# Optimization experiments

Hardware: AMD Instinct MI355X
Metric: run time of the kernel (lower is better)

The kernel has to match this reference:

```python
import jax, jax.numpy as jnp
import numpy as np

N = 50000


def gcn_conv(x, edge_index, W, b):
    # x: [N, F_in], edge_index: [2, E] (row=source j, col=target i)
    n = x.shape[0]
    loops = jnp.arange(n, dtype=edge_index.dtype)
    row = jnp.concatenate([edge_index[0], loops])
    col = jnp.concatenate([edge_index[1], loops])
    # linear transform first (PyG GCNConv)
    xw = x @ W  # [N, F_out]
    # symmetric normalization deg^{-1/2}[row] * deg^{-1/2}[col]
    deg = jax.ops.segment_sum(jnp.ones_like(col, dtype=xw.dtype), col, num_segments=n)
    dis = jnp.where(deg > 0, jax.lax.rsqrt(jnp.maximum(deg, 1e-12)), 0.0)
    norm = dis[row] * dis[col]  # [E+N]
    # gather-scale-scatter: sum_j norm_ij * (W x_j)
    msgs = xw[row] * norm[:, None]
    out = jax.ops.segment_sum(msgs, col, num_segments=n)
    return out + b


def setup_inputs() -> dict:
    key = jax.random.key(0)
    k1, k2, k3, k4, k5 = jax.random.split(key, 5)
    in_dim, hidden_dim, out_dim = 128, 128, 64
    x = jax.random.normal(k1, (N, in_dim), dtype=jnp.float32)
    edge_index = jax.random.randint(k2, (2, 800000), 0, N, dtype=jnp.int64)
    s1 = 1.0 / np.sqrt(in_dim)
    s2 = 1.0 / np.sqrt(hidden_dim)
    W1 = jax.random.uniform(k3, (in_dim, hidden_dim), jnp.float32, -s1, s1)
    b1 = jnp.zeros((hidden_dim,), jnp.float32)
    W2 = jax.random.uniform(k4, (hidden_dim, out_dim), jnp.float32, -s2, s2)
    b2 = jnp.zeros((out_dim,), jnp.float32)
    return {"x": x, "edge_index": edge_index, "W1": W1, "b1": b1, "W2": W2, "b2": b2}


def reference(x, edge_index, W1, b1, W2, b2):
    h = gcn_conv(x, edge_index, W1, b1)
    h = jax.nn.relu(h)
    # dropout(p=0.5, training=False) -> identity (inference reference)
    out = gcn_conv(h, edge_index, W2, b2)
    return out
```

## Files before the change

### kernel.cpp

```cpp
#include <hip/hip_runtime.h>
#include <hip/hip_fp16.h>


typedef _Float16 half8 __attribute__((ext_vector_type(8)));
typedef float floatx4 __attribute__((ext_vector_type(4)));

__global__ void k_count(const int* __restrict__ col, int* __restrict__ deg,
                        int* __restrict__ rank, int E) {
    int e = blockIdx.x * blockDim.x + threadIdx.x;
    if (e < E) rank[e] = atomicAdd(&deg[col[e]], 1);
}

__global__ __launch_bounds__(1024) void k_scan_local(const int* __restrict__ deg,
                                                     int* __restrict__ rowptr,
                                                     int* __restrict__ praw,
                                                     int* __restrict__ bsum,
                                                     float* __restrict__ dis, int n) {
    __shared__ int wsum[16];
    int b = blockIdx.x, tid = threadIdx.x;
    int lane = tid & 63, w = tid >> 6;
    int i = b * 1024 + tid;
    int v = (i < n) ? deg[i] : 0;
    if (i < n) dis[i] = rsqrtf((float)v + 1.0f);
    int sc = v;
#pragma unroll
    for (int off = 1; off < 64; off <<= 1) {
        int t = __shfl_up(sc, off);
        if (lane >= off) sc += t;
    }
    if (lane == 63) wsum[w] = sc;
    __syncthreads();
    if (w == 0) {
        int s = (lane < 16) ? wsum[lane] : 0;
#pragma unroll
        for (int off = 1; off < 16; off <<= 1) {
            int t = __shfl_up(s, off);
            if (lane >= off) s += t;
        }
        if (lane < 16) wsum[lane] = s;
    }
    __syncthreads();
    int incl = sc + ((w > 0) ? wsum[w - 1] : 0);
    if (i < n) {
        rowptr[i + 1] = incl;
        praw[i + 1] = incl;
    }
    if (tid == 1023) bsum[b] = incl;
    if (b == 0 && tid == 0) {
        rowptr[0] = 0;
        praw[0] = 0;
    }
}

template <int N, typename AT>
__device__ __forceinline__ void gemm_tile(const AT* __restrict__ X,
                                          const float* __restrict__ W,
                                          const float* __restrict__ scale,
                                          __half* __restrict__ Y, int M,
                                          int m0, __half2* wt, int tid) {
    for (int i = tid; i < N * 64; i += 256) {
        int nn = i & (N - 1);
        int k2 = i / N;
        float w0 = W[(size_t)(2 * k2) * N + nn];
        float w1 = W[(size_t)(2 * k2 + 1) * N + nn];
        wt[nn * 64 + ((k2 >> 2) ^ (nn & 15)) * 4 + (k2 & 3)] = __floats2half2_rn(w0, w1);
    }
    __syncthreads();
    int wid = tid >> 6, lane = tid & 63;
    int col = lane & 15, quad = lane >> 4;
    int m_a = m0 + wid * 16 + col;
    bool a_ok = m_a < M;
    constexpr int NT = N / 16;
    floatx4 acc[NT] = {};
#pragma unroll
    for (int ks = 0; ks < 4; ++ks) {
        int k = ks * 32 + quad * 8;
        half8 af;
        if constexpr (sizeof(AT) == 4) {
            floatx4 a0 = {0.f, 0.f, 0.f, 0.f}, a1 = {0.f, 0.f, 0.f, 0.f};
            if (a_ok) {
                a0 = *(const floatx4*)&X[(size_t)m_a * 128 + k];
                a1 = *(const floatx4*)&X[(size_t)m_a * 128 + k + 4];
            }
            af = half8{(_Float16)a0[0], (_Float16)a0[1], (_Float16)a0[2], (_Float16)a0[3],
                       (_Float16)a1[0], (_Float16)a1[1], (_Float16)a1[2], (_Float16)a1[3]};
        } else {
            half8 t = {};
            if (a_ok) t = *(const half8*)(const void*)&X[(size_t)m_a * 128 + k];
            af = t;
        }
        int kblk = ks * 4 + quad;
#pragma unroll
        for (int nt = 0; nt < NT; ++nt) {
            int nn = nt * 16 + col;
            half8 bf = *(const half8*)(const void*)&wt[nn * 64 + (kblk ^ (nn & 15)) * 4];
            acc[nt] = __builtin_amdgcn_mfma_f32_16x16x32_f16(af, bf, acc[nt], 0, 0, 0);
        }
    }
    int mbase = m0 + wid * 16 + quad * 4;
    float s[4];
#pragma unroll
    for (int r = 0; r < 4; ++r) s[r] = (mbase + r < M) ? scale[mbase + r] : 0.f;
#pragma unroll
    for (int nt = 0; nt < NT; ++nt) {
#pragma unroll
        for (int r = 0; r < 4; ++r) {
            if (mbase + r < M)
                Y[(size_t)(mbase + r) * N + nt * 16 + col] = __float2half(acc[nt][r] * s[r]);
        }
    }
}

__global__ __launch_bounds__(256) void k_fused(int* __restrict__ rowptr,
                                               const int* __restrict__ bsum, int n,
                                               const float* __restrict__ X,
                                               const float* __restrict__ W,
                                               const float* __restrict__ scale,
                                               __half* __restrict__ Y, int M,
                                               int FB, int GB,
                                               const int* __restrict__ praw,
                                               const int* __restrict__ row,
                                               const int* __restrict__ col,
                                               const int* __restrict__ rank,
                                               int* __restrict__ csr, int E) {
    __shared__ __align__(16) __half2 wt[128 * 64];
    int b = blockIdx.x, tid = threadIdx.x;
    if (b < FB) {
        int* red = (int*)wt;
        int partial = 0;
        for (int j = tid; j < b; j += 256) partial += bsum[j];
        red[tid] = partial;
        __syncthreads();
        for (int off = 128; off > 0; off >>= 1) {
            if (tid < off) red[tid] += red[tid + off];
            __syncthreads();
        }
        int offv = red[0];
        if (offv == 0) return;
#pragma unroll
        for (int r = 0; r < 4; ++r) {
            int i = b * 1024 + r * 256 + tid;
            if (i < n) rowptr[i + 1] += offv;
        }
        return;
    }
    if (b >= FB + GB) {
        int* q = (int*)wt;
        int nb = (n + 1023) >> 10;
        if (tid < 64) {
            int v = (tid >= 1 && tid <= nb) ? bsum[tid - 1] : 0;
#pragma unroll
            for (int off = 1; off < 64; off <<= 1) {
                int t = __shfl_up(v, off);
                if ((tid & 63) >= off) v += t;
            }
            q[tid] = v;
        }
        __syncthreads();
        int base = (b - FB - GB) * 1024;
#pragma unroll
        for (int r = 0; r < 4; ++r) {
            int e = base + r * 256 + tid;
            if (e < E) {
                int c = col[e];
                int qi = (c == 0) ? 0 : ((c - 1) >> 10);
                csr[praw[c] + q[qi] + rank[e]] = row[e];
            }
        }
        return;
    }
    gemm_tile<128, float>(X, W, scale, Y, M, (b - FB) * 64, wt, tid);
}

__global__ __launch_bounds__(256) void k_agg_gemm(const __half* __restrict__ xw,
                                                  const float* __restrict__ dis,
                                                  const int* __restrict__ rowptr,
                                                  const int* __restrict__ csr,
                                                  const float* __restrict__ bias,
                                                  const float* __restrict__ W2,
                                                  __half* __restrict__ Y,
                                                  int n) {
    __shared__ __align__(16) half8 htile[64 * 16];
    __shared__ __align__(16) __half2 wt[64 * 64];
    int tid = threadIdx.x, b = blockIdx.x;
    int lane = tid & 63, w = tid >> 6;
    int q = lane >> 4, li = lane & 15;
    int qbase = lane & 48;

    for (int i = tid; i < 64 * 64; i += 256) {
        int nn = i & 63;
        int k2 = i >> 6;
        float w0 = W2[(size_t)(2 * k2) * 64 + nn];
        float w1 = W2[(size_t)(2 * k2 + 1) * 64 + nn];
        wt[nn * 64 + ((k2 >> 2) ^ (nn & 15)) * 4 + (k2 & 3)] = __floats2half2_rn(w0, w1);
    }

    const half8* rows = (const half8*)xw;
    floatx4 bb0 = *(const floatx4*)&bias[li * 8];
    floatx4 bb1 = *(const floatx4*)&bias[li * 8 + 4];

#pragma unroll
    for (int g = 0; g < 4; ++g) {
        int m_loc = g * 16 + (w << 2) + q;
        int node = b * 64 + m_loc;
        bool ok = node < n;
        float di = 0.f;
        int beg = 0, end = 0;
        if (ok) {
            di = dis[node];
            beg = rowptr[node];
            end = rowptr[node + 1];
        }
        int dg = end - beg;
        int m1 = max(dg, __shfl(dg, lane ^ 16));
        int mx = max(m1, __shfl(m1, lane ^ 32));
        float acc[8] = {};
        if (ok) {
            half8 sf = rows[(size_t)node * 16 + li];
#pragma unroll
            for (int f = 0; f < 8; ++f) acc[f] = (float)sf[f];
        }
        for (int i = 0; i < mx; i += 8) {
            int e = beg + i + (li & 7);
            int myidx = (e < end) ? csr[e] : 0;
            half8 v[8];
#pragma unroll
            for (int j = 0; j < 8; ++j) {
                int s = __shfl(myidx, qbase + j);
                v[j] = rows[(size_t)s * 16 + li];
            }
#pragma unroll
            for (int j = 0; j < 8; ++j) {
                if (beg + i + j < end) {
#pragma unroll
                    for (int f = 0; f < 8; ++f) acc[f] += (float)v[j][f];
                }
            }
        }
        half8 o = {};
        if (ok) {
#pragma unroll
            for (int f = 0; f < 4; ++f) o[f] = (_Float16)fmaxf(acc[f] * di + bb0[f], 0.f);
#pragma unroll
            for (int f = 0; f < 4; ++f) o[4 + f] = (_Float16)fmaxf(acc[4 + f] * di + bb1[f], 0.f);
        }
        htile[m_loc * 16 + (li ^ (m_loc & 7))] = o;
    }
    __syncthreads();

    int col16 = lane & 15, quad = lane >> 4;
    int m_loc = w * 16 + col16;
    floatx4 gacc[4] = {};
#pragma unroll
    for (int ks = 0; ks < 4; ++ks) {
        half8 af = htile[m_loc * 16 + ((ks * 4 + quad) ^ (m_loc & 7))];
        int kblk = ks * 4 + quad;
#pragma unroll
        for (int nt = 0; nt < 4; ++nt) {
            int nn = nt * 16 + col16;
            half8 bf = *(const half8*)(const void*)&wt[nn * 64 + (kblk ^ (nn & 15)) * 4];
            gacc[nt] = __builtin_amdgcn_mfma_f32_16x16x32_f16(af, bf, gacc[nt], 0, 0, 0);
        }
    }
    int mbase = b * 64 + w * 16 + quad * 4;
    float s[4];
#pragma unroll
    for (int r = 0; r < 4; ++r) s[r] = (mbase + r < n) ? dis[mbase + r] : 0.f;
#pragma unroll
    for (int nt = 0; nt < 4; ++nt) {
#pragma unroll
        for (int r = 0; r < 4; ++r) {
            if (mbase + r < n)
                Y[(size_t)(mbase + r) * 64 + nt * 16 + col16] = __float2half(gacc[nt][r] * s[r]);
        }
    }
}

__global__ __launch_bounds__(256) void k_agg64(const __half* __restrict__ xw,
                                               const float* __restrict__ dis,
                                               const int* __restrict__ rowptr,
                                               const int* __restrict__ csr,
                                               const float* __restrict__ bias,
                                               float* __restrict__ out, int n) {
    int tid = threadIdx.x;
    int lane = tid & 63;
    int o8 = lane >> 3, li = lane & 7;
    int obase = lane & 56;
    int node = blockIdx.x * 32 + ((tid >> 6) << 3) + o8;
    bool ok = node < n;
    float di = 0.f;
    int beg = 0, end = 0;
    if (ok) {
        di = dis[node];
        beg = rowptr[node];
        end = rowptr[node + 1];
    }
    int dg = end - beg;
    int m1 = max(dg, __shfl(dg, lane ^ 8));
    int m2 = max(m1, __shfl(m1, lane ^ 16));
    int mx = max(m2, __shfl(m2, lane ^ 32));
    const half8* rows = (const half8*)xw;
    float acc[8] = {};
    if (ok) {
        half8 sf = rows[(size_t)node * 8 + li];
#pragma unroll
        for (int f = 0; f < 8; ++f) acc[f] = (float)sf[f];
    }
    for (int i = 0; i < mx; i += 8) {
        int e = beg + i + li;
        int myidx = (e < end) ? csr[e] : 0;
        half8 v[8];
#pragma unroll
        for (int j = 0; j < 8; ++j) {
            int s = __shfl(myidx, obase + j);
            v[j] = rows[(size_t)s * 8 + li];
        }
#pragma unroll
        for (int j = 0; j < 8; ++j) {
            if (beg + i + j < end) {
#pragma unroll
                for (int f = 0; f < 8; ++f) acc[f] += (float)v[j][f];
            }
        }
    }
    if (ok) {
        floatx4 b0 = *(const floatx4*)&bias[li * 8];
        floatx4 b1 = *(const floatx4*)&bias[li * 8 + 4];
        floatx4 o0, o1;
#pragma unroll
        for (int f = 0; f < 4; ++f) o0[f] = acc[f] * di + b0[f];
#pragma unroll
        for (int f = 0; f < 4; ++f) o1[f] = acc[4 + f] * di + b1[f];
        *(floatx4*)&out[(size_t)node * 64 + li * 8] = o0;
        *(floatx4*)&out[(size_t)node * 64 + li * 8 + 4] = o1;
    }
}

extern "C" void kernel_launch(void* const* d_in, const int* in_sizes, int n_in,
                              void* d_out, int out_size, void* d_ws, size_t ws_size,
                              hipStream_t stream) {
    const float* x  = (const float*)d_in[0];
    const int*   ei = (const int*)d_in[1];
    const float* W1 = (const float*)d_in[2];
    const float* b1 = (const float*)d_in[3];
    const float* W2 = (const float*)d_in[4];
    const float* b2 = (const float*)d_in[5];
    float* out = (float*)d_out;

    const int n = in_sizes[0] / 128;
    const int E = in_sizes[1] / 2;
    const int* row = ei;
    const int* col = ei + E;
    const int NB = (n + 1023) / 1024;
    const int CB = (E + 255) / 256;
    const int GB = (n + 63) / 64;
    const int FILLB = (E + 1023) / 1024;

    char* ws = (char*)d_ws;
    size_t off = 0;
    auto alloc = [&](size_t bytes) -> void* {
        void* p = ws + off;
        off += (bytes + 255) & ~(size_t)255;
        return p;
    };
    int*    deg    = (int*)alloc((size_t)n * 4);
    int*    rowptr = (int*)alloc((size_t)(n + 1) * 4);
    int*    praw   = (int*)alloc((size_t)(n + 1) * 4);
    int*    bsum   = (int*)alloc((size_t)NB * 4);
    int*    rank   = (int*)alloc((size_t)E * 4);
    int*    csr    = (int*)alloc((size_t)E * 4);
    float*  dis    = (float*)alloc((size_t)n * 4);
    __half* xw1    = (__half*)alloc((size_t)n * 128 * 2);
    __half* xw2    = (__half*)alloc((size_t)n * 64 * 2);
    (void)ws_size;

    hipMemsetAsync(deg, 0, (size_t)n * 4, stream);
    k_count<<<CB, 256, 0, stream>>>(col, deg, rank, E);
    k_scan_local<<<NB, 1024, 0, stream>>>(deg, rowptr, praw, bsum, dis, n);
    k_fused<<<NB + GB + FILLB, 256, 0, stream>>>(rowptr, bsum, n, x, W1, dis, xw1,
                                                 n, NB, GB, praw, row, col, rank,
                                                 csr, E);
    k_agg_gemm<<<GB, 256, 0, stream>>>(xw1, dis, rowptr, csr, b1, W2, xw2, n);
    k_agg64<<<(n + 31) / 32, 256, 0, stream>>>(xw2, dis, rowptr, csr, b2, out, n);
}
```

Before: 198.8 us.

## Merge degree count, scan, CSR fill and first GEMM into one cooperative kernel

Replaces the memset, count, local scan and fused fix/fill/GEMM launches with a single cooperative kernel that uses grid-wide syncs between phases. The scan now handles 1024 nodes per block with 4 elements per thread, and the final phase splits the persistent grid by fixed ratios into rowptr fix, CSR fill and GEMM roles. This is meant to remove launch overhead and inter-kernel gaps. In exchange it adds four grid barriers and a fixed role split that can leave the GEMM or fill phase underprovisioned, and it assumes no more than 64 scan chunks.

Result: slower. 477.6 us (+140.2%).

```diff
diff --git a/kernel.cpp b/kernel.cpp
--- a/kernel.cpp
+++ b/kernel.cpp
@@ -1,63 +1,16 @@
 #include <hip/hip_runtime.h>
 #include <hip/hip_fp16.h>
+#include <hip/hip_cooperative_groups.h>
+
+namespace cg = cooperative_groups;
 
 
 typedef _Float16 half8 __attribute__((ext_vector_type(8)));
 typedef float floatx4 __attribute__((ext_vector_type(4)));
 
-__global__ void k_count(const int* __restrict__ col, int* __restrict__ deg,
-                        int* __restrict__ rank, int E) {
-    int e = blockIdx.x * blockDim.x + threadIdx.x;
-    if (e < E) rank[e] = atomicAdd(&deg[col[e]], 1);
-}
-
-__global__ __launch_bounds__(1024) void k_scan_local(const int* __restrict__ deg,
-                                                     int* __restrict__ rowptr,
-                                                     int* __restrict__ praw,
-                                                     int* __restrict__ bsum,
-                                                     float* __restrict__ dis, int n) {
-    __shared__ int wsum[16];
-    int b = blockIdx.x, tid = threadIdx.x;
-    int lane = tid & 63, w = tid >> 6;
-    int i = b * 1024 + tid;
-    int v = (i < n) ? deg[i] : 0;
-    if (i < n) dis[i] = rsqrtf((float)v + 1.0f);
-    int sc = v;
-#pragma unroll
-    for (int off = 1; off < 64; off <<= 1) {
-        int t = __shfl_up(sc, off);
-        if (lane >= off) sc += t;
-    }
-    if (lane == 63) wsum[w] = sc;
-    __syncthreads();
-    if (w == 0) {
-        int s = (lane < 16) ? wsum[lane] : 0;
-#pragma unroll
-        for (int off = 1; off < 16; off <<= 1) {
-            int t = __shfl_up(s, off);
-            if (lane >= off) s += t;
-        }
-        if (lane < 16) wsum[lane] = s;
-    }
-    __syncthreads();
-    int incl = sc + ((w > 0) ? wsum[w - 1] : 0);
-    if (i < n) {
-        rowptr[i + 1] = incl;
-        praw[i + 1] = incl;
-    }
-    if (tid == 1023) bsum[b] = incl;
-    if (b == 0 && tid == 0) {
-        rowptr[0] = 0;
-        praw[0] = 0;
-    }
-}
-
-template <int N, typename AT>
-__device__ __forceinline__ void gemm_tile(const AT* __restrict__ X,
-                                          const float* __restrict__ W,
-                                          const float* __restrict__ scale,
-                                          __half* __restrict__ Y, int M,
-                                          int m0, __half2* wt, int tid) {
+template <int N>
+__device__ __forceinline__ void stage_w(const float* __restrict__ W,
+                                        __half2* wt, int tid) {
     for (int i = tid; i < N * 64; i += 256) {
         int nn = i & (N - 1);
         int k2 = i / N;
@@ -65,33 +18,30 @@
         float w1 = W[(size_t)(2 * k2 + 1) * N + nn];
         wt[nn * 64 + ((k2 >> 2) ^ (nn & 15)) * 4 + (k2 & 3)] = __floats2half2_rn(w0, w1);
     }
-    __syncthreads();
+}
+
+__device__ __forceinline__ void tile128(const float* __restrict__ X,
+                                        const float* __restrict__ scale,
+                                        __half* __restrict__ Y, int M,
+                                        int m0, const __half2* wt, int tid) {
     int wid = tid >> 6, lane = tid & 63;
     int col = lane & 15, quad = lane >> 4;
     int m_a = m0 + wid * 16 + col;
     bool a_ok = m_a < M;
-    constexpr int NT = N / 16;
-    floatx4 acc[NT] = {};
+    floatx4 acc[8] = {};
 #pragma unroll
     for (int ks = 0; ks < 4; ++ks) {
         int k = ks * 32 + quad * 8;
-        half8 af;
-        if constexpr (sizeof(AT) == 4) {
-            floatx4 a0 = {0.f, 0.f, 0.f, 0.f}, a1 = {0.f, 0.f, 0.f, 0.f};
-            if (a_ok) {
-                a0 = *(const floatx4*)&X[(size_t)m_a * 128 + k];
-                a1 = *(const floatx4*)&X[(size_t)m_a * 128 + k + 4];
-            }
-            af = half8{(_Float16)a0[0], (_Float16)a0[1], (_Float16)a0[2], (_Float16)a0[3],
-                       (_Float16)a1[0], (_Float16)a1[1], (_Float16)a1[2], (_Float16)a1[3]};
-        } else {
-            half8 t = {};
-            if (a_ok) t = *(const half8*)(const void*)&X[(size_t)m_a * 128 + k];
-            af = t;
-        }
+        floatx4 a0 = {0.f, 0.f, 0.f, 0.f}, a1 = {0.f, 0.f, 0.f, 0.f};
+        if (a_ok) {
+            a0 = *(const floatx4*)&X[(size_t)m_a * 128 + k];
+            a1 = *(const floatx4*)&X[(size_t)m_a * 128 + k + 4];
+        }
+        half8 af = half8{(_Float16)a0[0], (_Float16)a0[1], (_Float16)a0[2], (_Float16)a0[3],
+                         (_Float16)a1[0], (_Float16)a1[1], (_Float16)a1[2], (_Float16)a1[3]};
         int kblk = ks * 4 + quad;
 #pragma unroll
-        for (int nt = 0; nt < NT; ++nt) {
+        for (int nt = 0; nt < 8; ++nt) {
             int nn = nt * 16 + col;
             half8 bf = *(const half8*)(const void*)&wt[nn * 64 + (kblk ^ (nn & 15)) * 4];
             acc[nt] = __builtin_amdgcn_mfma_f32_16x16x32_f16(af, bf, acc[nt], 0, 0, 0);
@@ -102,74 +52,118 @@
 #pragma unroll
     for (int r = 0; r < 4; ++r) s[r] = (mbase + r < M) ? scale[mbase + r] : 0.f;
 #pragma unroll
-    for (int nt = 0; nt < NT; ++nt) {
+    for (int nt = 0; nt < 8; ++nt) {
 #pragma unroll
         for (int r = 0; r < 4; ++r) {
             if (mbase + r < M)
-                Y[(size_t)(mbase + r) * N + nt * 16 + col] = __float2half(acc[nt][r] * s[r]);
-        }
-    }
-}
-
-__global__ __launch_bounds__(256) void k_fused(int* __restrict__ rowptr,
-                                               const int* __restrict__ bsum, int n,
-                                               const float* __restrict__ X,
-                                               const float* __restrict__ W,
-                                               const float* __restrict__ scale,
-                                               __half* __restrict__ Y, int M,
-                                               int FB, int GB,
-                                               const int* __restrict__ praw,
-                                               const int* __restrict__ row,
-                                               const int* __restrict__ col,
-                                               const int* __restrict__ rank,
-                                               int* __restrict__ csr, int E) {
+                Y[(size_t)(mbase + r) * 128 + nt * 16 + col] = __float2half(acc[nt][r] * s[r]);
+        }
+    }
+}
+
+__global__ __launch_bounds__(256, 4) void k_coop(int* __restrict__ rowptr,
+                                                 int* __restrict__ praw,
+                                                 int* __restrict__ bsum,
+                                                 int* __restrict__ qpre,
+                                                 int* __restrict__ deg,
+                                                 float* __restrict__ dis,
+                                                 int* __restrict__ rank,
+                                                 int* __restrict__ csr,
+                                                 const float* __restrict__ x,
+                                                 const float* __restrict__ W1,
+                                                 __half* __restrict__ xw1,
+                                                 const int* __restrict__ row,
+                                                 const int* __restrict__ col,
+                                                 int n, int E, int NCH) {
     __shared__ __align__(16) __half2 wt[128 * 64];
+    __shared__ int wsum[4];
+    cg::grid_group grid = cg::this_grid();
     int b = blockIdx.x, tid = threadIdx.x;
-    if (b < FB) {
-        int* red = (int*)wt;
-        int partial = 0;
-        for (int j = tid; j < b; j += 256) partial += bsum[j];
-        red[tid] = partial;
+    int G = gridDim.x;
+    int gid = b * 256 + tid, gsz = G * 256;
+    int lane = tid & 63, w = tid >> 6;
+
+    for (int i = gid; i < n; i += gsz) deg[i] = 0;
+    grid.sync();
+
+    for (int e = gid; e < E; e += gsz) rank[e] = atomicAdd(&deg[col[e]], 1);
+    grid.sync();
+
+    if (b < NCH) {
+        int i0 = b * 1024 + tid * 4;
+        int lv[4], tsum = 0;
+        float dv[4];
+#pragma unroll
+        for (int r = 0; r < 4; ++r) {
+            int idx = i0 + r;
+            int d = (idx < n) ? deg[idx] : 0;
+            tsum += d;
+            lv[r] = tsum;
+            dv[r] = rsqrtf((float)d + 1.0f);
+        }
+        int sc = tsum;
+#pragma unroll
+        for (int off = 1; off < 64; off <<= 1) {
+            int t = __shfl_up(sc, off);
+            if (lane >= off) sc += t;
+        }
+        if (lane == 63) wsum[w] = sc;
         __syncthreads();
-        for (int off = 128; off > 0; off >>= 1) {
-            if (tid < off) red[tid] += red[tid + off];
-            __syncthreads();
-        }
-        int offv = red[0];
-        if (offv == 0) return;
+        int wpre = 0;
+#pragma unroll
+        for (int j = 0; j < 4; ++j)
+            if (j < w) wpre += wsum[j];
+        int texcl = wpre + sc - tsum;
 #pragma unroll
         for (int r = 0; r < 4; ++r) {
-            int i = b * 1024 + r * 256 + tid;
-            if (i < n) rowptr[i + 1] += offv;
-        }
-        return;
-    }
-    if (b >= FB + GB) {
-        int* q = (int*)wt;
-        int nb = (n + 1023) >> 10;
+            int idx = i0 + r;
+            if (idx < n) {
+                praw[idx + 1] = texcl + lv[r];
+                dis[idx] = dv[r];
+            }
+        }
+        if (tid == 255) bsum[b] = wpre + sc;
+    }
+    grid.sync();
+
+    if (b == 0) {
         if (tid < 64) {
-            int v = (tid >= 1 && tid <= nb) ? bsum[tid - 1] : 0;
+            int val = (tid < NCH) ? bsum[tid] : 0;
+            int s = val;
 #pragma unroll
             for (int off = 1; off < 64; off <<= 1) {
-                int t = __shfl_up(v, off);
-                if ((tid & 63) >= off) v += t;
-            }
-            q[tid] = v;
-        }
+                int t = __shfl_up(s, off);
+                if ((tid & 63) >= off) s += t;
+            }
+            qpre[tid] = s - val;
+        }
+        if (tid == 0) praw[0] = 0;
+    }
+    grid.sync();
+
+    int FIXB = G >> 4;
+    int GEMB = (3 * G) >> 4;
+    int FILLB = G - FIXB - GEMB;
+    if (b < FIXB) {
+        for (int j = b * 256 + tid; j <= n; j += FIXB * 256)
+            rowptr[j] = (j == 0) ? 0 : praw[j] + qpre[(j - 1) >> 10];
+    } else if (b < FIXB + FILLB) {
+        int* qlds = (int*)wt;
+        if (tid < 64) qlds[tid] = qpre[tid];
         __syncthreads();
-        int base = (b - FB - GB) * 1024;
-#pragma unroll
-        for (int r = 0; r < 4; ++r) {
-            int e = base + r * 256 + tid;
-            if (e < E) {
-                int c = col[e];
-                int qi = (c == 0) ? 0 : ((c - 1) >> 10);
-                csr[praw[c] + q[qi] + rank[e]] = row[e];
-            }
-        }
-        return;
-    }
-    gemm_tile<128, float>(X, W, scale, Y, M, (b - FB) * 64, wt, tid);
+        int bb = b - FIXB;
+        for (int e = bb * 256 + tid; e < E; e += FILLB * 256) {
+            int c = col[e];
+            int q0 = (c == 0) ? 0 : qlds[(c - 1) >> 10];
+            csr[praw[c] + q0 + rank[e]] = row[e];
+        }
+    } else {
+        stage_w<128>(W1, wt, tid);
+        __syncthreads();
+        int NT1 = (n + 63) >> 6;
+        for (int t = b - FIXB - FILLB; t < NT1; t += GEMB)
+            tile128(x, dis, xw1, n, t * 64, wt, tid);
+    }
 }
 
 __global__ __launch_bounds__(256) void k_agg_gemm(const __half* __restrict__ xw,
@@ -347,14 +341,12 @@
     const float* b2 = (const float*)d_in[5];
     float* out = (float*)d_out;
 
-    const int n = in_sizes[0] / 128;
-    const int E = in_sizes[1] / 2;
+    int n = in_sizes[0] / 128;
+    int E = in_sizes[1] / 2;
     const int* row = ei;
     const int* col = ei + E;
-    const int NB = (n + 1023) / 1024;
-    const int CB = (E + 255) / 256;
+    int NCH = (n + 1023) / 1024;
     const int GB = (n + 63) / 64;
-    const int FILLB = (E + 1023) / 1024;
 
     char* ws = (char*)d_ws;
     size_t off = 0;
@@ -366,7 +358,8 @@
     int*    deg    = (int*)alloc((size_t)n * 4);
     int*    rowptr = (int*)alloc((size_t)(n + 1) * 4);
     int*    praw   = (int*)alloc((size_t)(n + 1) * 4);
-    int*    bsum   = (int*)alloc((size_t)NB * 4);
+    int*    bsum   = (int*)alloc((size_t)64 * 4);
+    int*    qpre   = (int*)alloc((size_t)64 * 4);
     int*    rank   = (int*)alloc((size_t)E * 4);
     int*    csr    = (int*)alloc((size_t)E * 4);
     float*  dis    = (float*)alloc((size_t)n * 4);
@@ -374,12 +367,20 @@
     __half* xw2    = (__half*)alloc((size_t)n * 64 * 2);
     (void)ws_size;
 
-    hipMemsetAsync(deg, 0, (size_t)n * 4, stream);
-    k_count<<<CB, 256, 0, stream>>>(col, deg, rank, E);
-    k_scan_local<<<NB, 1024, 0, stream>>>(deg, rowptr, praw, bsum, dis, n);
-    k_fused<<<NB + GB + FILLB, 256, 0, stream>>>(rowptr, bsum, n, x, W1, dis, xw1,
-                                                 n, NB, GB, praw, row, col, rank,
-                                                 csr, E);
+    int G = 1024;
+    int maxb = 0;
+    if (hipOccupancyMaxActiveBlocksPerMultiprocessor(&maxb, k_coop, 256, 0) == hipSuccess &&
+        maxb > 0) {
+        int cap = maxb * 256;
+        if (G > cap) G = cap;
+    }
+    if (G < 64) G = 64;
+
+    void* cargs[] = {&rowptr, &praw, &bsum, &qpre, &deg, &dis, &rank, &csr,
+                     (void*)&x, (void*)&W1, &xw1, (void*)&row, (void*)&col,
+                     &n, &E, &NCH};
+    hipLaunchCooperativeKernel((const void*)k_coop, dim3(G), dim3(256), cargs, 0, stream);
+
     k_agg_gemm<<<GB, 256, 0, stream>>>(xw1, dis, rowptr, csr, b1, W2, xw2, n);
     k_agg64<<<(n + 31) / 32, 256, 0, stream>>>(xw2, dis, rowptr, csr, b2, out, n);
 }
```
